# Optimization experiments

Hardware: AMD Instinct MI355X
Metric: run time of the kernel (lower is better)

The kernel has to match this reference:

```python
import jax, jax.numpy as jnp
import numpy as np

B, N, D, H, R = 4, 4096, 1024, 16, 64
HD = D // H  # head_dim = 64


def setup_inputs() -> dict:
    key = jax.random.key(0)
    ks = jax.random.split(key, 8)
    x = jax.random.normal(ks[0], (B, N, D), dtype=jnp.float32)
    # nn.Linear weights are (out, in); y = x @ W.T
    Wq = jax.random.normal(ks[1], (D, D), dtype=jnp.float32) * (1.0 / np.sqrt(D))
    Wk = jax.random.normal(ks[2], (D, D), dtype=jnp.float32) * (1.0 / np.sqrt(D))
    Wv = jax.random.normal(ks[3], (D, D), dtype=jnp.float32) * (1.0 / np.sqrt(D))
    Wo = jax.random.normal(ks[4], (D, D), dtype=jnp.float32) * (1.0 / np.sqrt(D))
    bo = jnp.zeros((D,), dtype=jnp.float32)
    E = jax.random.normal(ks[5], (N, R), dtype=jnp.float32) * 0.02
    Fm = jax.random.normal(ks[6], (N, R), dtype=jnp.float32) * 0.02
    return {"x": x, "Wq": Wq, "Wk": Wk, "Wv": Wv, "Wo": Wo, "bo": bo, "E": E, "Fm": Fm}


def reference(x, Wq, Wk, Wv, Wo, bo, E, Fm):
    b, n, d = x.shape
    scale = np.sqrt(HD).astype(np.float32)
    # projections: torch Linear => x @ W.T ; reshape to (B, H, N, HD)
    def proj(W):
        y = jnp.einsum('bnd,ed->bne', x, W)
        return y.reshape(b, n, H, HD).transpose(0, 2, 1, 3)
    Q = proj(Wq)  # (B,H,N,HD)
    K = proj(Wk)
    V = proj(Wv)
    # low-rank projections along sequence: (B,H,R,HD)
    K_low = jnp.einsum('nr,bhnd->bhrd', E[:n], K)
    V_low = jnp.einsum('nr,bhnd->bhrd', Fm[:n], V)
    scores = jnp.einsum('bhnd,bhrd->bhnr', Q, K_low) / scale  # (B,H,N,R)
    attn = jax.nn.softmax(scores, axis=-1)
    out = jnp.einsum('bhnr,bhrd->bhnd', attn, V_low)  # (B,H,N,HD)
    out = out.transpose(0, 2, 1, 3).reshape(b, n, d)
    return jnp.einsum('bnd,ed->bne', out, Wo) + bo
```

## Files before the change

kernel.cpp:

```cpp
#include <hip/hip_runtime.h>
#include <stdint.h>

typedef __bf16 bf16;
typedef __bf16 bf16x8 __attribute__((ext_vector_type(8)));
typedef __bf16 bf16x4 __attribute__((ext_vector_type(4)));
typedef float  f32x4  __attribute__((ext_vector_type(4)));

#define NB   4096
#define DB   1024
#define RV   64
#define MB   16384
#define NSEG 8

__global__ void detect_dtype(const unsigned short* x, int* flag) {
  __shared__ int cnt;
  if (threadIdx.x == 0) cnt = 0;
  __syncthreads();
  int local = 0;
  for (int i = threadIdx.x; i < 8192; i += 256) {
    const int e = (x[i] >> 7) & 0xFF;
    if (e >= 0xC0) local++;
  }
  atomicAdd(&cnt, local);
  __syncthreads();
  if (threadIdx.x == 0) *flag = (cnt > 64) ? 1 : 0;
}

struct CvtArgs {
  const void* src[8];
  bf16* dst[8];
  int n[8];
  int off[9];
};
__global__ void to_bf16_multi(CvtArgs a, const int* __restrict__ flag) {
  const int blk = blockIdx.x;
  int seg = 0;
#pragma unroll
  for (int s = 1; s < 8; ++s) seg += (blk >= a.off[s]);
  const int i = (blk - a.off[seg]) * 2048 + threadIdx.x * 8;
  if (i >= a.n[seg]) return;
  bf16* dst = a.dst[seg];
  if (*flag) {
    const float* s = (const float*)a.src[seg] + i;
    f32x4 x0 = *(const f32x4*)s;
    f32x4 x1 = *(const f32x4*)(s + 4);
    bf16x8 v;
    v[0]=(bf16)x0[0]; v[1]=(bf16)x0[1]; v[2]=(bf16)x0[2]; v[3]=(bf16)x0[3];
    v[4]=(bf16)x1[0]; v[5]=(bf16)x1[1]; v[6]=(bf16)x1[2]; v[7]=(bf16)x1[3];
    *(bf16x8*)(dst + i) = v;
  } else {
    *(uint4*)(dst + i) = *(const uint4*)((const bf16*)a.src[seg] + i);
  }
}

__global__ __launch_bounds__(256) void ef_transpose(
    const void* __restrict__ E, const void* __restrict__ F,
    bf16* __restrict__ EFt, const int* __restrict__ flag) {
  const int m = blockIdx.x;
  const int z = m >> 6, r = m & 63;
  const void* src = z ? F : E;
  const int t = threadIdx.x;
  bf16* dst = EFt + (size_t)m * 4096;
  if (*flag) {
    const float* s = (const float*)src;
#pragma unroll
    for (int i = 0; i < 16; ++i) {
      const int n = i*256 + t;
      dst[n] = (bf16)s[(size_t)n*RV + r];
    }
  } else {
    const bf16* s = (const bf16*)src;
#pragma unroll
    for (int i = 0; i < 16; ++i) {
      const int n = i*256 + t;
      dst[n] = s[(size_t)n*RV + r];
    }
  }
}

typedef __attribute__((address_space(1))) const void g_as1_void;
typedef __attribute__((address_space(3))) void as3_void;
static __device__ __forceinline__ void gload16(const void* g, void* l) {
  __builtin_amdgcn_global_load_lds((g_as1_void*)g, (as3_void*)l, 16, 0, 0);
}

__global__ __launch_bounds__(256, 4) void lowrank_mfma(
    const bf16* __restrict__ EFt, const bf16* __restrict__ xb,
    float* __restrict__ Pf) {
  const int b = blockIdx.x, dt = blockIdx.y, seg = blockIdx.z;
  __shared__ __align__(16) bf16 sEF0[128*64];
  __shared__ __align__(16) bf16 sEF1[128*64];
  __shared__ __align__(16) bf16 sXT[32*64];
  const int t = threadIdx.x, lane = t & 63, w = t >> 6;
  const int lr = lane & 15, quad = lane >> 4;
  const int wm = (w & 1) * 64, wd = (w >> 1) * 16;
  const int nbase = seg * (NB / NSEG);

  const bf16* gA[4];
  int abase[4];
#pragma unroll
  for (int i = 0; i < 4; ++i) {
    const int c = i*256 + t, row = c >> 3, ch = c & 7;
    gA[i] = EFt + (size_t)row*4096 + nbase + (ch ^ (row & 7))*8;
    abase[i] = (i*256 + (w << 6)) * 8;
  }
  const bf16* gx = xb + ((size_t)b*NB + nbase + lane)*DB + dt*32 + w*8;
  int xslot[8];
#pragma unroll
  for (int j = 0; j < 8; ++j) {
    const int d = w*8 + j;
    xslot[j] = (d*8 + ((lane >> 3) ^ (d & 7)))*8 + (lane & 7);
  }
  f32x4 acc[4] = {};

  uint4 rx = *(const uint4*)gx;
#pragma unroll
  for (int i = 0; i < 4; ++i) gload16(gA[i], sEF0 + abase[i]);
  asm volatile("s_waitcnt vmcnt(0)" ::: "memory");
  __syncthreads();

  for (int kt = 0; kt < NB/NSEG; kt += 64) {
    {
      const bf16* px = (const bf16*)&rx;
#pragma unroll
      for (int j = 0; j < 8; ++j) sXT[xslot[j]] = px[j];
    }
    bf16* nbuf = ((kt >> 6) & 1) ? sEF0 : sEF1;
    if (kt + 64 < NB/NSEG) {
#pragma unroll
      for (int i = 0; i < 4; ++i) gload16(gA[i] + kt + 64, nbuf + abase[i]);
      rx = *(const uint4*)(gx + (size_t)(kt + 64)*DB);
    }
    asm volatile("s_waitcnt lgkmcnt(0)" ::: "memory");
    __syncthreads();
    const bf16* cbuf = ((kt >> 6) & 1) ? sEF1 : sEF0;
#pragma unroll
    for (int ks = 0; ks < 2; ++ks) {
      const int kc = ks*4 + quad;
      const int dd = wd + lr;
      bf16x8 bv = *(const bf16x8*)(sXT + (dd*8 + (kc ^ (dd & 7)))*8);
#pragma unroll
      for (int mi = 0; mi < 4; ++mi) {
        const int m = wm + mi*16 + lr;
        bf16x8 af = *(const bf16x8*)(cbuf + (m*8 + (kc ^ (m & 7)))*8);
        acc[mi] = __builtin_amdgcn_mfma_f32_16x16x32_bf16(af, bv, acc[mi], 0, 0, 0);
      }
    }
    if (kt + 64 < NB/NSEG) asm volatile("s_waitcnt vmcnt(1)" ::: "memory");
    __syncthreads();
  }

  float* dst = Pf + (((size_t)seg*4 + b)*128)*DB + dt*32 + wd + lr;
#pragma unroll
  for (int mi = 0; mi < 4; ++mi) {
    const int row128 = wm + mi*16 + quad*4;
#pragma unroll
    for (int rg = 0; rg < 4; ++rg)
      dst[(size_t)(row128 + rg)*DB] = acc[mi][rg];
  }
}

__global__ __launch_bounds__(256) void lowrank_reduce(
    const float* __restrict__ Pf, bf16* __restrict__ xEb, bf16* __restrict__ xFb) {
  const int idx = blockIdx.x*256 + threadIdx.x;
  const int d4  = idx & 255;
  const int row = (idx >> 8) & 127;
  const int b   = idx >> 15;
  const float* p = Pf + ((size_t)b*128 + row)*DB + d4*4;
  f32x4 s = {};
#pragma unroll
  for (int seg = 0; seg < NSEG; ++seg) {
    f32x4 v = *(const f32x4*)(p + (size_t)seg*4*128*DB);
    s[0]+=v[0]; s[1]+=v[1]; s[2]+=v[2]; s[3]+=v[3];
  }
  bf16x4 o;
  o[0]=(bf16)s[0]; o[1]=(bf16)s[1]; o[2]=(bf16)s[2]; o[3]=(bf16)s[3];
  bf16* dst = (row < 64 ? xEb : xFb) + ((size_t)b*64 + (row & 63))*DB + d4*4;
  *(bf16x4*)dst = o;
}

struct GemmArgs {
  const bf16* A;
  const bf16* B;
  void* C;
  const bf16* bias;
  const int* oflag;
  int force_f32;
  int M, N, K;
  const bf16* A2;
  const bf16* B2;
  void* C2;
  int dual;
};

__global__ __launch_bounds__(256, 4) void gemm_nt(GemmArgs args) {
  const int K = args.K, N = args.N;
  const bf16* Aptr = args.A;
  const bf16* Bptr = args.B;
  void* Cptr = args.C;
  if (args.dual && blockIdx.z == 1) { Aptr = args.A2; Bptr = args.B2; Cptr = args.C2; }
  __shared__ __align__(16) char smem[32768];
  bf16* const sA = (bf16*)smem;
  bf16* const sB = (bf16*)(smem + 16384);

  const int t = threadIdx.x;
  const int lane = t & 63;
  const int w = t >> 6;
  const int lr = lane & 15;
  const int quad = lane >> 4;
  const int wm = (w & 1) * 64;
  const int wn = (w >> 1) * 64;

  int bx = blockIdx.x, by = blockIdx.y;
  if (gridDim.y == 128) {
    const int l = by * 8 + bx;
    const int xcd = l & 7, s = l >> 3;
    by = xcd * 16 + (s >> 3);
    bx = s & 7;
  }
  const int m0 = by * 128;
  const int n0 = bx * 128;

  const bf16* gA[4];
  const bf16* gB[4];
  int lds_off[4];
#pragma unroll
  for (int i = 0; i < 4; ++i) {
    const int c = i*256 + t;
    const int row = c >> 3, ch = c & 7;
    const int sc = ch ^ (row & 7);
    gA[i] = Aptr + (size_t)(m0 + row)*K + sc*8;
    gB[i] = Bptr + (size_t)(n0 + row)*K + sc*8;
    lds_off[i] = (i*256 + w*64) * 8;
  }

  f32x4 acc[4][4] = {};

  for (int kt = 0; kt < K; kt += 64) {
    __syncthreads();
#pragma unroll
    for (int i = 0; i < 4; ++i) gload16(gA[i] + kt, sA + lds_off[i]);
#pragma unroll
    for (int i = 0; i < 4; ++i) gload16(gB[i] + kt, sB + lds_off[i]);
    __syncthreads();
#pragma unroll
    for (int ks = 0; ks < 2; ++ks) {
      const int kc = ks*4 + quad;
      bf16x8 af[4], bv[4];
#pragma unroll
      for (int mi = 0; mi < 4; ++mi) {
        const int m = wm + mi*16 + lr;
        af[mi] = *(const bf16x8*)(sA + (m*8 + (kc ^ (m & 7)))*8);
      }
#pragma unroll
      for (int ni = 0; ni < 4; ++ni) {
        const int n = wn + ni*16 + lr;
        bv[ni] = *(const bf16x8*)(sB + (n*8 + (kc ^ (n & 7)))*8);
      }
#pragma unroll
      for (int mi = 0; mi < 4; ++mi)
#pragma unroll
        for (int ni = 0; ni < 4; ++ni)
          acc[mi][ni] = __builtin_amdgcn_mfma_f32_16x16x32_bf16(
              af[mi], bv[ni], acc[mi][ni], 0, 0, 0);
    }
  }

  __syncthreads();

  const int f32out = args.force_f32 | (args.oflag ? *args.oflag : 0);
  float* sEw = (float*)(smem + w * 8192);
#pragma unroll
  for (int hh = 0; hh < 2; ++hh) {
    if (hh) asm volatile("s_waitcnt lgkmcnt(0)" ::: "memory");
#pragma unroll
    for (int mi2 = 0; mi2 < 2; ++mi2) {
      const int mi = hh*2 + mi2;
#pragma unroll
      for (int ni = 0; ni < 4; ++ni) {
        const int colg = n0 + wn + ni*16 + lr;
        const float bvv = args.bias ? (float)args.bias[colg] : 0.0f;
#pragma unroll
        for (int rg = 0; rg < 4; ++rg) {
          const int row = mi2*16 + quad*4 + rg;
          sEw[row*64 + ((ni*16 + lr) ^ ((row & 15)*4))] = acc[mi][ni][rg] + bvv;
        }
      }
    }
    asm volatile("s_waitcnt lgkmcnt(0)" ::: "memory");
#pragma unroll
    for (int i = 0; i < 4; ++i) {
      const int c = i*64 + lane;
      const int row = c >> 3, ch = c & 7;
      const int d0 = ch * 8;
      const int swz = (row & 15) * 4;
      f32x4 v0 = *(const f32x4*)(sEw + row*64 + (d0 ^ swz));
      f32x4 v1 = *(const f32x4*)(sEw + row*64 + ((d0 + 4) ^ swz));
      const size_t base = (size_t)(m0 + wm + hh*32 + row)*N + n0 + wn + d0;
      if (f32out) {
        *(f32x4*)((float*)Cptr + base)     = v0;
        *(f32x4*)((float*)Cptr + base + 4) = v1;
      } else {
        bf16x8 wv;
        wv[0]=(bf16)v0[0]; wv[1]=(bf16)v0[1]; wv[2]=(bf16)v0[2]; wv[3]=(bf16)v0[3];
        wv[4]=(bf16)v1[0]; wv[5]=(bf16)v1[1]; wv[6]=(bf16)v1[2]; wv[7]=(bf16)v1[3];
        *(bf16x8*)((bf16*)Cptr + base) = wv;
      }
    }
  }
}

__global__ __launch_bounds__(256, 2) void attn_mfma(
    const bf16* Q, const float* __restrict__ Klow,
    const float* __restrict__ Vlow, bf16* AO) {
  const int bh = blockIdx.x, b = bh >> 4, h = bh & 15;
  const int n0 = blockIdx.y * 128;

  __shared__ bf16 sQ[128*64];
  __shared__ bf16 sKb[64*64];
  __shared__ bf16 sVt[64*64];
  __shared__ bf16 sP[4][32*64];

  const int t = threadIdx.x;
  const int lane = t & 63;
  const int w = t >> 6;
  const int lr = lane & 15;
  const int quad = lane >> 4;

#pragma unroll
  for (int i = 0; i < 4; ++i) {
    const int c = i*256 + t;
    const int row = c >> 3, j = c & 7;
    const uint4 v = *(const uint4*)(Q + ((size_t)b*NB + n0 + row)*DB + h*64 + j*8);
    *(uint4*)(sQ + (row*8 + (j ^ (row & 7)))*8) = v;
  }
  {
    const int r = t >> 2, c0 = (t & 3) * 16;
    const float* kb = Klow + (size_t)(b*64 + r)*DB + h*64 + c0;
    const float* vb = Vlow + (size_t)(b*64 + r)*DB + h*64 + c0;
    float kf[16], vf[16];
#pragma unroll
    for (int i = 0; i < 4; ++i) {
      *(f32x4*)(kf + i*4) = *(const f32x4*)(kb + i*4);
      *(f32x4*)(vf + i*4) = *(const f32x4*)(vb + i*4);
    }
#pragma unroll
    for (int cc = 0; cc < 2; ++cc) {
      bf16x8 pk;
#pragma unroll
      for (int j2 = 0; j2 < 8; ++j2) pk[j2] = (bf16)kf[cc*8 + j2];
      const int ch = (c0 >> 3) + cc;
      *(bf16x8*)(sKb + (r*8 + (ch ^ (r & 7)))*8) = pk;
    }
#pragma unroll
    for (int j2 = 0; j2 < 16; ++j2) {
      const int d = c0 + j2;
      sVt[d*64 + (((r >> 3) ^ (d & 7))*8) + (r & 7)] = (bf16)vf[j2];
    }
  }
  __syncthreads();

  f32x4 accS[2][4] = {};
#pragma unroll
  for (int ks = 0; ks < 2; ++ks) {
    const int kc = ks*4 + quad;
    bf16x8 af[2], bv[4];
#pragma unroll
    for (int mi = 0; mi < 2; ++mi) {
      const int m = w*32 + mi*16 + lr;
      af[mi] = *(const bf16x8*)(sQ + (m*8 + (kc ^ (m & 7)))*8);
    }
#pragma unroll
    for (int ni = 0; ni < 4; ++ni) {
      const int r = ni*16 + lr;
      bv[ni] = *(const bf16x8*)(sKb + (r*8 + (kc ^ (r & 7)))*8);
    }
#pragma unroll
    for (int mi = 0; mi < 2; ++mi)
#pragma unroll
      for (int ni = 0; ni < 4; ++ni)
        accS[mi][ni] = __builtin_amdgcn_mfma_f32_16x16x32_bf16(
            af[mi], bv[ni], accS[mi][ni], 0, 0, 0);
  }

  float inv_[2][4];
#pragma unroll
  for (int mi = 0; mi < 2; ++mi)
#pragma unroll
    for (int rg = 0; rg < 4; ++rg) {
      float mv = -3.0e38f;
#pragma unroll
      for (int ni = 0; ni < 4; ++ni) mv = fmaxf(mv, accS[mi][ni][rg]);
#pragma unroll
      for (int d = 1; d < 16; d <<= 1) mv = fmaxf(mv, __shfl_xor(mv, d));
      float sum = 0.0f;
#pragma unroll
      for (int ni = 0; ni < 4; ++ni) {
        const float p = __expf((accS[mi][ni][rg] - mv) * 0.125f);
        accS[mi][ni][rg] = p;
        sum += p;
      }
#pragma unroll
      for (int d = 1; d < 16; d <<= 1) sum += __shfl_xor(sum, d);
      inv_[mi][rg] = 1.0f / sum;
    }

  bf16* myP = sP[w];
#pragma unroll
  for (int mi = 0; mi < 2; ++mi)
#pragma unroll
    for (int ni = 0; ni < 4; ++ni)
#pragma unroll
      for (int rg = 0; rg < 4; ++rg) {
        const int row = mi*16 + quad*4 + rg;
        const int col = ni*16 + lr;
        myP[row*64 + ((col >> 3) ^ (row & 7))*8 + (col & 7)] = (bf16)accS[mi][ni][rg];
      }

  f32x4 accO[2][4] = {};
#pragma unroll
  for (int ks = 0; ks < 2; ++ks) {
    const int kc = ks*4 + quad;
    bf16x8 ap[2], bvv[4];
#pragma unroll
    for (int mi = 0; mi < 2; ++mi) {
      const int m = mi*16 + lr;
      ap[mi] = *(const bf16x8*)(myP + (m*8 + (kc ^ (m & 7)))*8);
    }
#pragma unroll
    for (int di = 0; di < 4; ++di) {
      const int d = di*16 + lr;
      bvv[di] = *(const bf16x8*)(sVt + (d*8 + (kc ^ (d & 7)))*8);
    }
#pragma unroll
    for (int mi = 0; mi < 2; ++mi)
#pragma unroll
      for (int di = 0; di < 4; ++di)
        accO[mi][di] = __builtin_amdgcn_mfma_f32_16x16x32_bf16(
            ap[mi], bvv[di], accO[mi][di], 0, 0, 0);
  }

#pragma unroll
  for (int mi = 0; mi < 2; ++mi)
#pragma unroll
    for (int di = 0; di < 4; ++di)
#pragma unroll
      for (int rg = 0; rg < 4; ++rg) {
        const int row = mi*16 + quad*4 + rg;
        const int col = di*16 + lr;
        myP[row*64 + ((col >> 3) ^ (row & 7))*8 + (col & 7)] =
            (bf16)(accO[mi][di][rg] * inv_[mi][rg]);
      }
  asm volatile("s_waitcnt lgkmcnt(0)" ::: "memory");
#pragma unroll
  for (int i = 0; i < 4; ++i) {
    const int c = i*64 + lane;
    const int row = c >> 3, ch = c & 7;
    const bf16x8 v = *(const bf16x8*)(myP + row*64 + ((ch ^ (row & 7))*8));
    *(bf16x8*)(AO + ((size_t)b*NB + n0 + w*32 + row)*DB + h*64 + ch*8) = v;
  }
}

extern "C" void kernel_launch(void* const* d_in, const int* in_sizes, int n_in,
                              void* d_out, int out_size, void* d_ws, size_t ws_size,
                              hipStream_t stream) {
  char* ws = (char*)d_ws;
  const size_t MiB = 1024*1024;
  int*   flag = (int*)ws;
  float* Klow = (float*)(ws + 1*MiB);
  float* Vlow = (float*)(ws + 2*MiB);
  bf16*  xEb  = (bf16*)(ws + 3*MiB);
  bf16*  xFb  = (bf16*)(ws + 3*MiB + 512*1024);
  bf16*  EFt  = (bf16*)(ws + 4*MiB);
  bf16*  Wqb  = (bf16*)(ws + 7*MiB);
  bf16*  Wkb  = (bf16*)(ws + 9*MiB);
  bf16*  Wvb  = (bf16*)(ws + 11*MiB);
  bf16*  Wob  = (bf16*)(ws + 13*MiB);
  bf16*  bob  = (bf16*)(ws + 15*MiB);
  bf16*  xb   = (bf16*)(ws + 20*MiB);
  bf16*  S0   = (bf16*)(ws + 52*MiB);
  float* Pf   = (float*)(ws + 52*MiB);

  detect_dtype<<<1, 256, 0, stream>>>((const unsigned short*)d_in[0], flag);

  ef_transpose<<<dim3(128), 256, 0, stream>>>(d_in[6], d_in[7], EFt, flag);

  CvtArgs ca;
  bf16* dsts[6] = {xb, Wqb, Wkb, Wvb, Wob, bob};
  int   ns[6]   = {16777216, 1048576, 1048576, 1048576, 1048576, 1024};
  int off = 0;
  for (int i = 0; i < 6; ++i) {
    ca.src[i] = d_in[i]; ca.dst[i] = dsts[i]; ca.n[i] = ns[i];
    ca.off[i] = off; off += (ns[i] + 2047) / 2048;
  }
  for (int i = 6; i < 8; ++i) {
    ca.src[i] = d_in[0]; ca.dst[i] = xb; ca.n[i] = 0; ca.off[i] = off;
  }
  ca.off[8] = off;
  to_bf16_multi<<<dim3(off), 256, 0, stream>>>(ca, flag);

  lowrank_mfma<<<dim3(4, 32, NSEG), 256, 0, stream>>>(EFt, xb, Pf);
  lowrank_reduce<<<dim3(512), 256, 0, stream>>>(Pf, xEb, xFb);

  GemmArgs ka;
  ka.A = xEb; ka.B = Wkb; ka.C = Klow;
  ka.A2 = xFb; ka.B2 = Wvb; ka.C2 = Vlow;
  ka.dual = 1;
  ka.bias = nullptr; ka.oflag = nullptr; ka.force_f32 = 1;
  ka.M = 256; ka.N = DB; ka.K = DB;
  gemm_nt<<<dim3(8, 2, 2), 256, 0, stream>>>(ka);

  GemmArgs qa;
  qa.A = xb; qa.B = Wqb; qa.C = S0; qa.bias = nullptr;
  qa.oflag = nullptr; qa.force_f32 = 0;
  qa.A2 = nullptr; qa.B2 = nullptr; qa.C2 = nullptr; qa.dual = 0;
  qa.M = MB; qa.N = DB; qa.K = DB;
  gemm_nt<<<dim3(8, 128, 1), 256, 0, stream>>>(qa);

  attn_mfma<<<dim3(64, 32), 256, 0, stream>>>(S0, Klow, Vlow, S0);

  GemmArgs oa;
  oa.A = S0; oa.B = Wob; oa.C = d_out; oa.bias = bob;
  oa.oflag = flag; oa.force_f32 = 0;
  oa.A2 = nullptr; oa.B2 = nullptr; oa.C2 = nullptr; oa.dual = 0;
  oa.M = MB; oa.N = DB; oa.K = DB;
  gemm_nt<<<dim3(8, 128, 1), 256, 0, stream>>>(oa);
}
```

Baseline: 289.0 us.

## Fuse low-rank attention into the Q projection GEMM epilogue

The Q projection GEMM now runs the low-rank attention in its epilogue. Each wave's 64x64 tile (one head) is staged in shared memory, multiplied against Klow with a softmax, then multiplied against Vlow, and only the attention output is written. This drops the separate attention kernel and the write and read of Q through global memory. In exchange, Klow and Vlow are read as fp32 directly from global memory per wave, and the V loads are strided scalar accesses without any shared-memory staging. Register pressure in the GEMM also rises, which may hurt occupancy.

```diff
diff --git a/kernel.cpp b/kernel.cpp
--- a/kernel.cpp
+++ b/kernel.cpp
@@ -191,6 +191,9 @@
   const bf16* B2;
   void* C2;
   int dual;
+  const float* Klow;
+  const float* Vlow;
+  int fuse_attn;
 };
 
 __global__ __launch_bounds__(256, 4) void gemm_nt(GemmArgs args) {
@@ -267,6 +270,138 @@
   }
 
   __syncthreads();
+
+  if (args.fuse_attn) {
+    const int b = m0 >> 12;
+    const int h = (n0 + wn) >> 6;
+    bf16* patch = (bf16*)(smem + w * 8192);
+
+#pragma unroll
+    for (int mi = 0; mi < 4; ++mi)
+#pragma unroll
+      for (int ni = 0; ni < 4; ++ni)
+#pragma unroll
+        for (int rg = 0; rg < 4; ++rg) {
+          const int row = mi*16 + quad*4 + rg;
+          const int col = ni*16 + lr;
+          patch[row*64 + ((col >> 3) ^ (row & 7))*8 + (col & 7)] =
+              (bf16)acc[mi][ni][rg];
+        }
+
+    const float* Kb = args.Klow + (size_t)(b*64)*DB + h*64;
+    f32x4 accS[4][4] = {};
+#pragma unroll
+    for (int ks = 0; ks < 2; ++ks) {
+      const int kc = ks*4 + quad;
+      bf16x8 af[4], bv[4];
+#pragma unroll
+      for (int mi = 0; mi < 4; ++mi) {
+        const int m = mi*16 + lr;
+        af[mi] = *(const bf16x8*)(patch + (m*8 + (kc ^ (m & 7)))*8);
+      }
+#pragma unroll
+      for (int ni = 0; ni < 4; ++ni) {
+        const int r = ni*16 + lr;
+        f32x4 k0 = *(const f32x4*)(Kb + (size_t)r*DB + kc*8);
+        f32x4 k1 = *(const f32x4*)(Kb + (size_t)r*DB + kc*8 + 4);
+        bf16x8 kv;
+        kv[0]=(bf16)k0[0]; kv[1]=(bf16)k0[1]; kv[2]=(bf16)k0[2]; kv[3]=(bf16)k0[3];
+        kv[4]=(bf16)k1[0]; kv[5]=(bf16)k1[1]; kv[6]=(bf16)k1[2]; kv[7]=(bf16)k1[3];
+        bv[ni] = kv;
+      }
+#pragma unroll
+      for (int mi = 0; mi < 4; ++mi)
+#pragma unroll
+        for (int ni = 0; ni < 4; ++ni)
+          accS[mi][ni] = __builtin_amdgcn_mfma_f32_16x16x32_bf16(
+              af[mi], bv[ni], accS[mi][ni], 0, 0, 0);
+    }
+
+    float inv_[4][4];
+#pragma unroll
+    for (int mi = 0; mi < 4; ++mi)
+#pragma unroll
+      for (int rg = 0; rg < 4; ++rg) {
+        float mv = -3.0e38f;
+#pragma unroll
+        for (int ni = 0; ni < 4; ++ni) mv = fmaxf(mv, accS[mi][ni][rg]);
+#pragma unroll
+        for (int d = 1; d < 16; d <<= 1) mv = fmaxf(mv, __shfl_xor(mv, d));
+        float sum = 0.0f;
+#pragma unroll
+        for (int ni = 0; ni < 4; ++ni) {
+          const float p = __expf((accS[mi][ni][rg] - mv) * 0.125f);
+          accS[mi][ni][rg] = p;
+          sum += p;
+        }
+#pragma unroll
+        for (int d = 1; d < 16; d <<= 1) sum += __shfl_xor(sum, d);
+        inv_[mi][rg] = 1.0f / sum;
+      }
+
+    asm volatile("s_waitcnt lgkmcnt(0)" ::: "memory");
+#pragma unroll
+    for (int mi = 0; mi < 4; ++mi)
+#pragma unroll
+      for (int ni = 0; ni < 4; ++ni)
+#pragma unroll
+        for (int rg = 0; rg < 4; ++rg) {
+          const int row = mi*16 + quad*4 + rg;
+          const int col = ni*16 + lr;
+          patch[row*64 + ((col >> 3) ^ (row & 7))*8 + (col & 7)] =
+              (bf16)accS[mi][ni][rg];
+        }
+
+    const float* Vb = args.Vlow + (size_t)(b*64)*DB + h*64;
+    f32x4 accO[4][4] = {};
+#pragma unroll
+    for (int ks = 0; ks < 2; ++ks) {
+      const int kc = ks*4 + quad;
+      bf16x8 ap[4], bvv[4];
+#pragma unroll
+      for (int mi = 0; mi < 4; ++mi) {
+        const int m = mi*16 + lr;
+        ap[mi] = *(const bf16x8*)(patch + (m*8 + (kc ^ (m & 7)))*8);
+      }
+#pragma unroll
+      for (int di = 0; di < 4; ++di) {
+        const int d = di*16 + lr;
+        bf16x8 vv;
+#pragma unroll
+        for (int j = 0; j < 8; ++j)
+          vv[j] = (bf16)Vb[(size_t)(kc*8 + j)*DB + d];
+        bvv[di] = vv;
+      }
+#pragma unroll
+      for (int mi = 0; mi < 4; ++mi)
+#pragma unroll
+        for (int di = 0; di < 4; ++di)
+          accO[mi][di] = __builtin_amdgcn_mfma_f32_16x16x32_bf16(
+              ap[mi], bvv[di], accO[mi][di], 0, 0, 0);
+    }
+
+    asm volatile("s_waitcnt lgkmcnt(0)" ::: "memory");
+#pragma unroll
+    for (int mi = 0; mi < 4; ++mi)
+#pragma unroll
+      for (int di = 0; di < 4; ++di)
+#pragma unroll
+        for (int rg = 0; rg < 4; ++rg) {
+          const int row = mi*16 + quad*4 + rg;
+          const int col = di*16 + lr;
+          patch[row*64 + ((col >> 3) ^ (row & 7))*8 + (col & 7)] =
+              (bf16)(accO[mi][di][rg] * inv_[mi][rg]);
+        }
+    asm volatile("s_waitcnt lgkmcnt(0)" ::: "memory");
+#pragma unroll
+    for (int i = 0; i < 8; ++i) {
+      const int c = i*64 + lane;
+      const int row = c >> 3, ch = c & 7;
+      const bf16x8 v = *(const bf16x8*)(patch + row*64 + ((ch ^ (row & 7))*8));
+      *(bf16x8*)((bf16*)Cptr + (size_t)(m0 + wm + row)*N + h*64 + ch*8) = v;
+    }
+    return;
+  }
 
   const int f32out = args.force_f32 | (args.oflag ? *args.oflag : 0);
   float* sEw = (float*)(smem + w * 8192);
@@ -307,157 +442,6 @@
         *(bf16x8*)((bf16*)Cptr + base) = wv;
       }
     }
-  }
-}
-
-__global__ __launch_bounds__(256, 2) void attn_mfma(
-    const bf16* Q, const float* __restrict__ Klow,
-    const float* __restrict__ Vlow, bf16* AO) {
-  const int bh = blockIdx.x, b = bh >> 4, h = bh & 15;
-  const int n0 = blockIdx.y * 128;
-
-  __shared__ bf16 sQ[128*64];
-  __shared__ bf16 sKb[64*64];
-  __shared__ bf16 sVt[64*64];
-  __shared__ bf16 sP[4][32*64];
-
-  const int t = threadIdx.x;
-  const int lane = t & 63;
-  const int w = t >> 6;
-  const int lr = lane & 15;
-  const int quad = lane >> 4;
-
-#pragma unroll
-  for (int i = 0; i < 4; ++i) {
-    const int c = i*256 + t;
-    const int row = c >> 3, j = c & 7;
-    const uint4 v = *(const uint4*)(Q + ((size_t)b*NB + n0 + row)*DB + h*64 + j*8);
-    *(uint4*)(sQ + (row*8 + (j ^ (row & 7)))*8) = v;
-  }
-  {
-    const int r = t >> 2, c0 = (t & 3) * 16;
-    const float* kb = Klow + (size_t)(b*64 + r)*DB + h*64 + c0;
-    const float* vb = Vlow + (size_t)(b*64 + r)*DB + h*64 + c0;
-    float kf[16], vf[16];
-#pragma unroll
-    for (int i = 0; i < 4; ++i) {
-      *(f32x4*)(kf + i*4) = *(const f32x4*)(kb + i*4);
-      *(f32x4*)(vf + i*4) = *(const f32x4*)(vb + i*4);
-    }
-#pragma unroll
-    for (int cc = 0; cc < 2; ++cc) {
-      bf16x8 pk;
-#pragma unroll
-      for (int j2 = 0; j2 < 8; ++j2) pk[j2] = (bf16)kf[cc*8 + j2];
-      const int ch = (c0 >> 3) + cc;
-      *(bf16x8*)(sKb + (r*8 + (ch ^ (r & 7)))*8) = pk;
-    }
-#pragma unroll
-    for (int j2 = 0; j2 < 16; ++j2) {
-      const int d = c0 + j2;
-      sVt[d*64 + (((r >> 3) ^ (d & 7))*8) + (r & 7)] = (bf16)vf[j2];
-    }
-  }
-  __syncthreads();
-
-  f32x4 accS[2][4] = {};
-#pragma unroll
-  for (int ks = 0; ks < 2; ++ks) {
-    const int kc = ks*4 + quad;
-    bf16x8 af[2], bv[4];
-#pragma unroll
-    for (int mi = 0; mi < 2; ++mi) {
-      const int m = w*32 + mi*16 + lr;
-      af[mi] = *(const bf16x8*)(sQ + (m*8 + (kc ^ (m & 7)))*8);
-    }
-#pragma unroll
-    for (int ni = 0; ni < 4; ++ni) {
-      const int r = ni*16 + lr;
-      bv[ni] = *(const bf16x8*)(sKb + (r*8 + (kc ^ (r & 7)))*8);
-    }
-#pragma unroll
-    for (int mi = 0; mi < 2; ++mi)
-#pragma unroll
-      for (int ni = 0; ni < 4; ++ni)
-        accS[mi][ni] = __builtin_amdgcn_mfma_f32_16x16x32_bf16(
-            af[mi], bv[ni], accS[mi][ni], 0, 0, 0);
-  }
-
-  float inv_[2][4];
-#pragma unroll
-  for (int mi = 0; mi < 2; ++mi)
-#pragma unroll
-    for (int rg = 0; rg < 4; ++rg) {
-      float mv = -3.0e38f;
-#pragma unroll
-      for (int ni = 0; ni < 4; ++ni) mv = fmaxf(mv, accS[mi][ni][rg]);
-#pragma unroll
-      for (int d = 1; d < 16; d <<= 1) mv = fmaxf(mv, __shfl_xor(mv, d));
-      float sum = 0.0f;
-#pragma unroll
-      for (int ni = 0; ni < 4; ++ni) {
-        const float p = __expf((accS[mi][ni][rg] - mv) * 0.125f);
-        accS[mi][ni][rg] = p;
-        sum += p;
-      }
-#pragma unroll
-      for (int d = 1; d < 16; d <<= 1) sum += __shfl_xor(sum, d);
-      inv_[mi][rg] = 1.0f / sum;
-    }
-
-  bf16* myP = sP[w];
-#pragma unroll
-  for (int mi = 0; mi < 2; ++mi)
-#pragma unroll
-    for (int ni = 0; ni < 4; ++ni)
-#pragma unroll
-      for (int rg = 0; rg < 4; ++rg) {
-        const int row = mi*16 + quad*4 + rg;
-        const int col = ni*16 + lr;
-        myP[row*64 + ((col >> 3) ^ (row & 7))*8 + (col & 7)] = (bf16)accS[mi][ni][rg];
-      }
-
-  f32x4 accO[2][4] = {};
-#pragma unroll
-  for (int ks = 0; ks < 2; ++ks) {
-    const int kc = ks*4 + quad;
-    bf16x8 ap[2], bvv[4];
-#pragma unroll
-    for (int mi = 0; mi < 2; ++mi) {
-      const int m = mi*16 + lr;
-      ap[mi] = *(const bf16x8*)(myP + (m*8 + (kc ^ (m & 7)))*8);
-    }
-#pragma unroll
-    for (int di = 0; di < 4; ++di) {
-      const int d = di*16 + lr;
-      bvv[di] = *(const bf16x8*)(sVt + (d*8 + (kc ^ (d & 7)))*8);
-    }
-#pragma unroll
-    for (int mi = 0; mi < 2; ++mi)
-#pragma unroll
-      for (int di = 0; di < 4; ++di)
-        accO[mi][di] = __builtin_amdgcn_mfma_f32_16x16x32_bf16(
-            ap[mi], bvv[di], accO[mi][di], 0, 0, 0);
-  }
-
-#pragma unroll
-  for (int mi = 0; mi < 2; ++mi)
-#pragma unroll
-    for (int di = 0; di < 4; ++di)
-#pragma unroll
-      for (int rg = 0; rg < 4; ++rg) {
-        const int row = mi*16 + quad*4 + rg;
-        const int col = di*16 + lr;
-        myP[row*64 + ((col >> 3) ^ (row & 7))*8 + (col & 7)] =
-            (bf16)(accO[mi][di][rg] * inv_[mi][rg]);
-      }
-  asm volatile("s_waitcnt lgkmcnt(0)" ::: "memory");
-#pragma unroll
-  for (int i = 0; i < 4; ++i) {
-    const int c = i*64 + lane;
-    const int row = c >> 3, ch = c & 7;
-    const bf16x8 v = *(const bf16x8*)(myP + row*64 + ((ch ^ (row & 7))*8));
-    *(bf16x8*)(AO + ((size_t)b*NB + n0 + w*32 + row)*DB + h*64 + ch*8) = v;
   }
 }
 
@@ -508,6 +492,7 @@
   ka.dual = 1;
   ka.bias = nullptr; ka.oflag = nullptr; ka.force_f32 = 1;
   ka.M = 256; ka.N = DB; ka.K = DB;
+  ka.Klow = nullptr; ka.Vlow = nullptr; ka.fuse_attn = 0;
   gemm_nt<<<dim3(8, 2, 2), 256, 0, stream>>>(ka);
 
   GemmArgs qa;
@@ -515,14 +500,14 @@
   qa.oflag = nullptr; qa.force_f32 = 0;
   qa.A2 = nullptr; qa.B2 = nullptr; qa.C2 = nullptr; qa.dual = 0;
   qa.M = MB; qa.N = DB; qa.K = DB;
+  qa.Klow = Klow; qa.Vlow = Vlow; qa.fuse_attn = 1;
   gemm_nt<<<dim3(8, 128, 1), 256, 0, stream>>>(qa);
-
-  attn_mfma<<<dim3(64, 32), 256, 0, stream>>>(S0, Klow, Vlow, S0);
 
   GemmArgs oa;
   oa.A = S0; oa.B = Wob; oa.C = d_out; oa.bias = bob;
   oa.oflag = flag; oa.force_f32 = 0;
   oa.A2 = nullptr; oa.B2 = nullptr; oa.C2 = nullptr; oa.dual = 0;
   oa.M = MB; oa.N = DB; oa.K = DB;
+  oa.Klow = nullptr; oa.Vlow = nullptr; oa.fuse_attn = 0;
   gemm_nt<<<dim3(8, 128, 1), 256, 0, stream>>>(oa);
 }
```

New measurement: 399.9 us. 38.4% more time.
